# Performance work log

Hardware: AMD Instinct MI355X
Metric: run time of the kernel (lower is better)

## Reference

```python
import jax, jax.numpy as jnp
import numpy as np
from jax import lax

B_SZ, L, D, N, R = 1, 4096, 768, 16, 48  # R = dt_rank = ceil(D/16)


def _soft_clamp(x, lo=1e-4, hi=10.0):
    center = (hi + lo) / 2.0
    half_range = (hi - lo) / 2.0
    return center + half_range * jnp.tanh((x - center) / half_range)


def setup_inputs() -> dict:
    key = jax.random.key(0)
    ks = jax.random.split(key, 6)
    x = jax.random.normal(ks[0], (B_SZ, L, D), jnp.float32)
    # A_log init: log(1..N) broadcast over D (HiPPO-style S4D-real init)
    A_log = jnp.log(jnp.broadcast_to(jnp.arange(1, N + 1, dtype=jnp.float32), (D, N)))
    D_param = jnp.ones((D,), jnp.float32)
    # lecun_normal kernels
    W_bc = jax.random.normal(ks[1], (D, 2 * N), jnp.float32) / np.sqrt(D).astype(np.float32)
    W_dt = jax.random.normal(ks[2], (D, R), jnp.float32) / np.sqrt(D).astype(np.float32)
    W_dtp = jax.random.normal(ks[3], (R, D), jnp.float32) / np.sqrt(R).astype(np.float32)
    # dt bias init: inverse-softplus of uniform(dt_min, dt_max)
    dt = jax.random.uniform(ks[4], (D,), jnp.float32, 0.001, 0.1)
    dt = jnp.clip(dt, 1e-4)
    b_dt = dt + jnp.log(-jnp.expm1(-dt))
    rms_scale = jnp.ones((D,), jnp.float32)  # RMSNorm learnable scale
    return {"x": x, "A_log": A_log, "D_param": D_param, "W_bc": W_bc,
            "W_dt": W_dt, "W_dtp": W_dtp, "b_dt": b_dt, "rms_scale": rms_scale}


def reference(x, A_log, D_param, W_bc, W_dt, W_dtp, b_dt, rms_scale):
    n = A_log.shape[1]
    A = -jnp.exp(A_log)                                   # (D, N)
    bc = x @ W_bc                                         # (B, L, 2N)
    B_sel, C_sel = bc[..., :n], bc[..., n:]               # (B, L, N) each
    # delta = softplus(dt_proj(x_dt)) -> RMSNorm -> soft_clamp  (tustin mode)
    delta = jax.nn.softplus((x @ W_dt) @ W_dtp + b_dt)    # (B, L, D)
    delta = delta * lax.rsqrt(jnp.mean(delta * delta, axis=-1, keepdims=True) + 1e-6) * rms_scale
    delta = _soft_clamp(delta, 1e-4, 10.0)
    # Bilinear (Tustin) discretization, all fp32 already
    dE = delta[..., None]                                 # (B, L, D, 1)
    half = 0.5 * dE * A                                   # (B, L, D, N)
    denom = 1.0 - half
    A_bar = (1.0 + half) / denom                          # (B, L, D, N)
    B_bar = jnp.sqrt(dE) * B_sel[:, :, None, :] / denom   # (B, L, D, N)
    # trapezoidal input averaging
    x_prev = jnp.concatenate([jnp.zeros_like(x[:, :1]), x[:, :-1]], axis=1)
    x_in = 0.5 * (x + x_prev)                             # (B, L, D)
    Bx = B_bar * x_in[..., None]                          # (B, L, D, N)

    def op(left, right):
        a_l, b_l = left
        a_r, b_r = right
        return (a_r * a_l, a_r * b_l + b_r)

    _, all_h = lax.associative_scan(op, (A_bar, Bx), axis=1)
    y = jnp.sum(C_sel[:, :, None, :] * all_h, axis=-1)    # (B, L, D)
    return y + D_param * x
```

## Files before the change

kernel.cpp:

```cpp
#include <hip/hip_runtime.h>
#include <math.h>

#define LSEQ 4096
#define DD 768
#define NST 16
#define RNK 48
#define TCH 64
#define NCH (LSEQ / TCH)
#define KSTEPS 24
#define NTILES 5
#define WFRAG_N (KSTEPS * NTILES * 64 * 8)
#define WDTP_N  (2 * RNK * 64 * 8)

typedef __attribute__((ext_vector_type(8))) short bf16x8;
typedef __attribute__((ext_vector_type(4))) float f32x4;

__device__ __forceinline__ float softplus_f(float z) {
    float e = __expf(-fabsf(z));
    return fmaxf(z, 0.0f) + __logf(1.0f + e);
}

__device__ __forceinline__ float tanh_fast(float w) {
    float t = __expf(2.0f * fabsf(w));
    float r = 1.0f - 2.0f / (t + 1.0f);
    return copysignf(r, w);
}

__device__ __forceinline__ float soft_clamp_f(float v) {
    const float ctr = 5.00005f;
    const float hr  = 4.99995f;
    const float inv_hr = 1.0f / 4.99995f;
    return ctr + hr * tanh_fast((v - ctr) * inv_hr);
}

__device__ __forceinline__ float wave_sum(float v) {
    #pragma unroll
    for (int m = 32; m >= 1; m >>= 1) v += __shfl_xor(v, m, 64);
    return v;
}

__device__ __forceinline__ unsigned short rne_bf16(float v) {
    unsigned u = __float_as_uint(v);
    return (unsigned short)((u + 0x7FFFu + ((u >> 16) & 1u)) >> 16);
}

__global__ __launch_bounds__(256) void k_prep(
    const float* __restrict__ W_dt, const float* __restrict__ W_bc,
    const float* __restrict__ W_dtp,
    unsigned short* __restrict__ wf_hi, unsigned short* __restrict__ wf_lo,
    unsigned short* __restrict__ wp_hi, unsigned short* __restrict__ wp_lo)
{
    int i = blockIdx.x * 256 + threadIdx.x;
    if (i < WFRAG_N) {
        int j  = i & 7;
        int l  = (i >> 3) & 63;
        int nk = i >> 9;
        int n  = nk % NTILES;
        int kk = nk / NTILES;
        int k   = kk * 32 + (l >> 4) * 8 + j;
        int col = n * 16 + (l & 15);
        float v = (col < RNK) ? W_dt[k * RNK + col] : W_bc[k * 32 + (col - RNK)];
        unsigned short h = rne_bf16(v);
        float hf = __uint_as_float((unsigned)h << 16);
        wf_hi[i] = h;
        wf_lo[i] = rne_bf16(v - hf);
    } else if (i < WFRAG_N + WDTP_N) {
        int ii = i - WFRAG_N;
        int j  = ii & 7;
        int l  = (ii >> 3) & 63;
        int nk = ii >> 9;
        int n  = nk % RNK;
        int ks = nk / RNK;
        int k   = ks * 32 + (l >> 4) * 8 + j;
        int col = n * 16 + (l & 15);
        float v = (k < RNK) ? W_dtp[k * DD + col] : 0.f;
        unsigned short h = rne_bf16(v);
        float hf = __uint_as_float((unsigned)h << 16);
        wp_hi[ii] = h;
        wp_lo[ii] = rne_bf16(v - hf);
    }
}

__global__ __launch_bounds__(512) void k_proj_mfma(
    const float* __restrict__ x,
    const unsigned short* __restrict__ wf_hi,
    const unsigned short* __restrict__ wf_lo,
    const unsigned short* __restrict__ wp_hi,
    const unsigned short* __restrict__ wp_lo,
    const float* __restrict__ b_dt, const float* __restrict__ rms_scale,
    float* __restrict__ c0_out, float* __restrict__ c1_out,
    float* __restrict__ bc_out)
{
    __shared__ __align__(16) float smem_x[16 * 772];
    __shared__ __align__(16) float smem_sp[16 * 772];
    __shared__ __align__(16) float t_lds[16][RNK];
    __shared__ float red2[8][16];

    const int tid  = threadIdx.x;
    const int lane = tid & 63;
    const int wq   = tid >> 6;
    const int mt   = blockIdx.x;

    {
        const float4* xg = (const float4*)(x + (size_t)mt * 16 * DD);
        #pragma unroll 2
        for (int idx = tid; idx < 3072; idx += 512) {
            int r = idx / 192, c4 = idx - r * 192;
            *(float4*)&smem_x[r * 772 + c4 * 4] = xg[idx];
        }
    }
    __syncthreads();

    const int rloc = lane & 15;
    const int ko   = (lane >> 4) * 8;

    f32x4 acc[NTILES];
    #pragma unroll
    for (int n = 0; n < NTILES; ++n) acc[n] = (f32x4){0.f, 0.f, 0.f, 0.f};

    #pragma unroll
    for (int k3 = 0; k3 < 3; ++k3) {
        const int kk = wq * 3 + k3;
        const float* xp = &smem_x[rloc * 772 + kk * 32 + ko];
        float4 xa = *(const float4*)xp;
        float4 xb = *(const float4*)(xp + 4);
        float va[8] = {xa.x, xa.y, xa.z, xa.w, xb.x, xb.y, xb.z, xb.w};
        bf16x8 ah, al;
        #pragma unroll
        for (int j = 0; j < 8; ++j) {
            unsigned short h = rne_bf16(va[j]);
            float hf = __uint_as_float((unsigned)h << 16);
            ah[j] = (short)h;
            al[j] = (short)rne_bf16(va[j] - hf);
        }
        const int base = kk * (NTILES * 512) + lane * 8;
        #pragma unroll
        for (int n = 0; n < NTILES; ++n) {
            bf16x8 bh = *(const bf16x8*)(wf_hi + base + n * 512);
            bf16x8 bl = *(const bf16x8*)(wf_lo + base + n * 512);
            acc[n] = __builtin_amdgcn_mfma_f32_16x16x32_bf16(al, bh, acc[n], 0, 0, 0);
            acc[n] = __builtin_amdgcn_mfma_f32_16x16x32_bf16(ah, bl, acc[n], 0, 0, 0);
            acc[n] = __builtin_amdgcn_mfma_f32_16x16x32_bf16(ah, bh, acc[n], 0, 0, 0);
        }
    }
    __syncthreads();

    if (wq > 0) {
        float* red = smem_sp + ((wq - 1) * 64 + lane) * 20;
        #pragma unroll
        for (int n = 0; n < NTILES; ++n)
            #pragma unroll
            for (int r = 0; r < 4; ++r) red[n * 4 + r] = acc[n][r];
    }
    __syncthreads();
    if (wq == 0) {
        #pragma unroll
        for (int w = 0; w < 7; ++w) {
            const float* red = smem_sp + (w * 64 + lane) * 20;
            #pragma unroll
            for (int n = 0; n < NTILES; ++n)
                #pragma unroll
                for (int r = 0; r < 4; ++r) acc[n][r] += red[n * 4 + r];
        }
        const int r0 = (lane >> 4) * 4;
        const int cb = lane & 15;
        #pragma unroll
        for (int n = 0; n < 3; ++n)
            #pragma unroll
            for (int r = 0; r < 4; ++r)
                t_lds[r0 + r][n * 16 + cb] = acc[n][r];
        #pragma unroll
        for (int n = 3; n < 5; ++n)
            #pragma unroll
            for (int r = 0; r < 4; ++r)
                bc_out[(size_t)(mt * 16 + r0 + r) * 32 + (n - 3) * 16 + cb] = acc[n][r];
    }
    __syncthreads();

    bf16x8 tah[2], tal[2];
    #pragma unroll
    for (int ks = 0; ks < 2; ++ks) {
        const int kbase = ks * 32 + ko;
        float tv[8];
        #pragma unroll
        for (int j = 0; j < 8; ++j)
            tv[j] = (kbase + j < RNK) ? t_lds[rloc][kbase + j] : 0.f;
        #pragma unroll
        for (int j = 0; j < 8; ++j) {
            unsigned short h = rne_bf16(tv[j]);
            float hf = __uint_as_float((unsigned)h << 16);
            tah[ks][j] = (short)h;
            tal[ks][j] = (short)rne_bf16(tv[j] - hf);
        }
    }

    const int r0 = (lane >> 4) * 4;
    #pragma unroll
    for (int nn = 0; nn < 6; ++nn) {
        const int n = wq * 6 + nn;
        f32x4 z = (f32x4){0.f, 0.f, 0.f, 0.f};
        {
            const int b0 = n * 512 + lane * 8;
            bf16x8 bh = *(const bf16x8*)(wp_hi + b0);
            bf16x8 bl = *(const bf16x8*)(wp_lo + b0);
            z = __builtin_amdgcn_mfma_f32_16x16x32_bf16(tal[0], bh, z, 0, 0, 0);
            z = __builtin_amdgcn_mfma_f32_16x16x32_bf16(tah[0], bl, z, 0, 0, 0);
            z = __builtin_amdgcn_mfma_f32_16x16x32_bf16(tah[0], bh, z, 0, 0, 0);
        }
        {
            const int b1 = (RNK + n) * 512 + lane * 8;
            bf16x8 bh = *(const bf16x8*)(wp_hi + b1);
            bf16x8 bl = *(const bf16x8*)(wp_lo + b1);
            z = __builtin_amdgcn_mfma_f32_16x16x32_bf16(tal[1], bh, z, 0, 0, 0);
            z = __builtin_amdgcn_mfma_f32_16x16x32_bf16(tah[1], bl, z, 0, 0, 0);
            z = __builtin_amdgcn_mfma_f32_16x16x32_bf16(tah[1], bh, z, 0, 0, 0);
        }
        const int col = n * 16 + (lane & 15);
        const float bb = b_dt[col];
        #pragma unroll
        for (int r = 0; r < 4; ++r)
            smem_sp[(r0 + r) * 772 + col] = softplus_f(z[r] + bb);
    }
    __syncthreads();

    const int d0 = tid;
    const int d1 = tid + 512;
    const bool has2 = (tid < 256);
    {
        float sp0[16], sp1[16];
        #pragma unroll
        for (int li = 0; li < 16; ++li) {
            sp0[li] = smem_sp[li * 772 + d0];
            sp1[li] = has2 ? smem_sp[li * 772 + d1] : 0.f;
        }
        #pragma unroll
        for (int li = 0; li < 16; ++li) {
            float ss = wave_sum(sp0[li] * sp0[li] + sp1[li] * sp1[li]);
            if (lane == 0) red2[wq][li] = ss;
        }
        __syncthreads();
        float rs0 = rms_scale[d0];
        float rs1 = has2 ? rms_scale[d1] : 0.f;
        float xm0 = (mt > 0) ? x[(size_t)(mt * 16 - 1) * DD + d0] : 0.f;
        float xm1 = (has2 && mt > 0) ? x[(size_t)(mt * 16 - 1) * DD + d1] : 0.f;
        #pragma unroll
        for (int li = 0; li < 16; ++li) {
            float tot = 0.f;
            #pragma unroll
            for (int k = 0; k < 8; ++k) tot += red2[k][li];
            float inv = rsqrtf(tot * (1.0f / DD) + 1e-6f);
            size_t rowoff = (size_t)(mt * 16 + li) * DD;

            float dl0 = soft_clamp_f(sp0[li] * inv * rs0);
            float xl0 = smem_x[li * 772 + d0];
            float xp0 = (li == 0) ? xm0 : smem_x[(li - 1) * 772 + d0];
            c0_out[rowoff + d0] = 0.5f * dl0;
            c1_out[rowoff + d0] = sqrtf(dl0) * 0.5f * (xl0 + xp0);

            if (has2) {
                float dl1 = soft_clamp_f(sp1[li] * inv * rs1);
                float xl1 = smem_x[li * 772 + d1];
                float xp1 = (li == 0) ? xm1 : smem_x[(li - 1) * 772 + d1];
                c0_out[rowoff + d1] = 0.5f * dl1;
                c1_out[rowoff + d1] = sqrtf(dl1) * 0.5f * (xl1 + xp1);
            }
        }
    }
}

__global__ __launch_bounds__(256, 4) void k_scan1(
    const float* __restrict__ c0b, const float* __restrict__ c1b,
    const float* __restrict__ bc, const float* __restrict__ A_log,
    float* __restrict__ Pbuf, float* __restrict__ Hbuf)
{
    __shared__ __align__(16) float c0v[TCH * 64];
    __shared__ __align__(16) float c1v[TCH * 64];
    __shared__ __align__(16) float bs[TCH * 16];

    const int tid = threadIdx.x;
    const int db  = blockIdx.x * 64;
    const int c   = blockIdx.y;
    const int l0  = c * TCH;

    for (int i = tid; i < TCH * 16; i += 256) {
        int r = i >> 4, f = i & 15;
        *(float4*)&c0v[r * 64 + f * 4] =
            *(const float4*)&c0b[(size_t)(l0 + r) * DD + db + f * 4];
        *(float4*)&c1v[r * 64 + f * 4] =
            *(const float4*)&c1b[(size_t)(l0 + r) * DD + db + f * 4];
    }
    for (int i = tid; i < TCH * 4; i += 256) {
        int r = i >> 2, f = i & 3;
        *(float4*)&bs[r * 16 + f * 4] =
            *(const float4*)&bc[(size_t)(l0 + r) * 32 + f * 4];
    }

    const int lane = tid & 63;
    const int w    = tid >> 6;
    const int q    = lane >> 4;
    const int dlo  = (lane & 15) + w * 16;
    const int d    = db + dlo;

    float An[4];
    {
        float4 a = *(const float4*)&A_log[d * NST + q * 4];
        An[0] = -__expf(a.x); An[1] = -__expf(a.y);
        An[2] = -__expf(a.z); An[3] = -__expf(a.w);
    }
    __syncthreads();

    float h[4]  = {0.f, 0.f, 0.f, 0.f};
    float Pp[4] = {1.f, 1.f, 1.f, 1.f};

    #pragma unroll 4
    for (int ll = 0; ll < TCH; ++ll) {
        float c0 = c0v[ll * 64 + dlo];
        float c1 = c1v[ll * 64 + dlo];
        float4 Bc = *(const float4*)&bs[ll * 16 + q * 4];

        float dn0 = fmaf(-c0, An[0], 1.0f);
        float dn1 = fmaf(-c0, An[1], 1.0f);
        float dn2 = fmaf(-c0, An[2], 1.0f);
        float dn3 = fmaf(-c0, An[3], 1.0f);
        float m01 = dn0 * dn1, m23 = dn2 * dn3;
        float ip  = __builtin_amdgcn_rcpf(m01 * m23);
        float ip01 = ip * m23, ip23 = ip * m01;
        float iv0 = ip01 * dn1, iv1 = ip01 * dn0;
        float iv2 = ip23 * dn3, iv3 = ip23 * dn2;
        float t10 = 2.0f - dn0, t11 = 2.0f - dn1;
        float t12 = 2.0f - dn2, t13 = 2.0f - dn3;

        Pp[0] *= t10 * iv0;
        Pp[1] *= t11 * iv1;
        Pp[2] *= t12 * iv2;
        Pp[3] *= t13 * iv3;
        h[0] = fmaf(t10, h[0], c1 * Bc.x) * iv0;
        h[1] = fmaf(t11, h[1], c1 * Bc.y) * iv1;
        h[2] = fmaf(t12, h[2], c1 * Bc.z) * iv2;
        h[3] = fmaf(t13, h[3], c1 * Bc.w) * iv3;
    }
    #pragma unroll
    for (int n = 0; n < 4; ++n) {
        int idx = (c * NST + q * 4 + n) * DD + d;
        Pbuf[idx] = Pp[n];
        Hbuf[idx] = h[n];
    }
}

__global__ __launch_bounds__(64) void k_scan2(
    float* __restrict__ Pbuf, const float* __restrict__ Hbuf)
{
    const int s = blockIdx.x * 64 + threadIdx.x;
    const int d = s % DD;
    const int n = s / DD;
    const int stride = NST * DD;

    int idx = n * DD + d;
    int idx_pf = idx;
    float p[8], h[8];
    #pragma unroll
    for (int i = 0; i < 8; ++i) {
        p[i] = Pbuf[idx_pf];
        h[i] = Hbuf[idx_pf];
        idx_pf += stride;
    }

    float carry = 0.f;
    for (int g = 0; g < NCH / 8; ++g) {
        float pn[8], hn[8];
        if (g + 1 < NCH / 8) {
            #pragma unroll
            for (int i = 0; i < 8; ++i) {
                pn[i] = Pbuf[idx_pf];
                hn[i] = Hbuf[idx_pf];
                idx_pf += stride;
            }
        }
        #pragma unroll
        for (int i = 0; i < 8; ++i) {
            Pbuf[idx] = carry;
            carry = fmaf(p[i], carry, h[i]);
            idx += stride;
        }
        #pragma unroll
        for (int i = 0; i < 8; ++i) { p[i] = pn[i]; h[i] = hn[i]; }
    }
}

__global__ __launch_bounds__(256, 4) void k_scan3(
    const float* __restrict__ x, const float* __restrict__ c0b,
    const float* __restrict__ c1b, const float* __restrict__ bc,
    const float* __restrict__ A_log, const float* __restrict__ carryin,
    const float* __restrict__ D_param, float* __restrict__ out)
{
    __shared__ __align__(16) float c0v[TCH * 64];
    __shared__ __align__(16) float c1v[TCH * 64];
    __shared__ __align__(16) float bs[TCH * 32];

    const int tid = threadIdx.x;
    const int db  = blockIdx.x * 64;
    const int c   = blockIdx.y;
    const int l0  = c * TCH;

    for (int i = tid; i < TCH * 16; i += 256) {
        int r = i >> 4, f = i & 15;
        *(float4*)&c0v[r * 64 + f * 4] =
            *(const float4*)&c0b[(size_t)(l0 + r) * DD + db + f * 4];
        *(float4*)&c1v[r * 64 + f * 4] =
            *(const float4*)&c1b[(size_t)(l0 + r) * DD + db + f * 4];
    }
    for (int i = tid; i < TCH * 8; i += 256) {
        int r = i >> 3, f = i & 7;
        *(float4*)&bs[r * 32 + f * 4] =
            *(const float4*)&bc[(size_t)(l0 + r) * 32 + f * 4];
    }

    const int lane = tid & 63;
    const int w    = tid >> 6;
    const int q    = lane >> 4;
    const int dlo  = (lane & 15) + w * 16;
    const int d    = db + dlo;

    float An[4];
    {
        float4 a = *(const float4*)&A_log[d * NST + q * 4];
        An[0] = -__expf(a.x); An[1] = -__expf(a.y);
        An[2] = -__expf(a.z); An[3] = -__expf(a.w);
    }
    float h[4];
    #pragma unroll
    for (int n = 0; n < 4; ++n)
        h[n] = carryin[(c * NST + q * 4 + n) * DD + d];
    const float Dp = D_param[d];

    __syncthreads();

    float xv_n = x[(size_t)l0 * DD + d];
    #pragma unroll 4
    for (int ll = 0; ll < TCH; ++ll) {
        float xv = xv_n;
        const int lnx = (l0 + ll + 1 < LSEQ) ? l0 + ll + 1 : l0 + ll;
        xv_n = x[(size_t)lnx * DD + d];

        float c0 = c0v[ll * 64 + dlo];
        float c1 = c1v[ll * 64 + dlo];
        float4 Bc = *(const float4*)&bs[ll * 32 + q * 4];
        float4 Cc = *(const float4*)&bs[ll * 32 + 16 + q * 4];

        float dn0 = fmaf(-c0, An[0], 1.0f);
        float dn1 = fmaf(-c0, An[1], 1.0f);
        float dn2 = fmaf(-c0, An[2], 1.0f);
        float dn3 = fmaf(-c0, An[3], 1.0f);
        float m01 = dn0 * dn1, m23 = dn2 * dn3;
        float ip  = __builtin_amdgcn_rcpf(m01 * m23);
        float ip01 = ip * m23, ip23 = ip * m01;
        float iv0 = ip01 * dn1, iv1 = ip01 * dn0;
        float iv2 = ip23 * dn3, iv3 = ip23 * dn2;
        float t10 = 2.0f - dn0, t11 = 2.0f - dn1;
        float t12 = 2.0f - dn2, t13 = 2.0f - dn3;

        h[0] = fmaf(t10, h[0], c1 * Bc.x) * iv0;
        h[1] = fmaf(t11, h[1], c1 * Bc.y) * iv1;
        h[2] = fmaf(t12, h[2], c1 * Bc.z) * iv2;
        h[3] = fmaf(t13, h[3], c1 * Bc.w) * iv3;

        float y = h[0] * Cc.x;
        y = fmaf(h[1], Cc.y, y);
        y = fmaf(h[2], Cc.z, y);
        y = fmaf(h[3], Cc.w, y);

        y += __shfl_xor(y, 16, 64);
        y += __shfl_xor(y, 32, 64);
        if (q == 0)
            out[(size_t)(l0 + ll) * DD + d] = fmaf(Dp, xv, y);
    }
}

extern "C" void kernel_launch(void* const* d_in, const int* in_sizes, int n_in,
                              void* d_out, int out_size, void* d_ws, size_t ws_size,
                              hipStream_t stream) {
    const float* x         = (const float*)d_in[0];
    const float* A_log     = (const float*)d_in[1];
    const float* D_param   = (const float*)d_in[2];
    const float* W_bc      = (const float*)d_in[3];
    const float* W_dt      = (const float*)d_in[4];
    const float* W_dtp     = (const float*)d_in[5];
    const float* b_dt      = (const float*)d_in[6];
    const float* rms_scale = (const float*)d_in[7];
    float* out = (float*)d_out;

    float* ws    = (float*)d_ws;
    float* c0buf = ws;
    float* c1buf = c0buf + (size_t)LSEQ * DD;
    float* bcbuf = c1buf + (size_t)LSEQ * DD;
    float* Pbuf  = bcbuf + (size_t)LSEQ * 32;
    float* Hbuf  = Pbuf + (size_t)NCH * NST * DD;
    unsigned short* wf_hi = (unsigned short*)(Hbuf + (size_t)NCH * NST * DD);
    unsigned short* wf_lo = wf_hi + WFRAG_N;
    unsigned short* wp_hi = wf_lo + WFRAG_N;
    unsigned short* wp_lo = wp_hi + WDTP_N;

    k_prep<<<(WFRAG_N + WDTP_N + 255) / 256, 256, 0, stream>>>(
        W_dt, W_bc, W_dtp, wf_hi, wf_lo, wp_hi, wp_lo);
    k_proj_mfma<<<LSEQ / 16, 512, 0, stream>>>(x, wf_hi, wf_lo, wp_hi, wp_lo,
                                               b_dt, rms_scale, c0buf, c1buf,
                                               bcbuf);
    k_scan1<<<dim3(DD / 64, NCH), 256, 0, stream>>>(c0buf, c1buf, bcbuf, A_log,
                                                    Pbuf, Hbuf);
    k_scan2<<<(DD * NST) / 64, 64, 0, stream>>>(Pbuf, Hbuf);
    k_scan3<<<dim3(DD / 64, NCH), 256, 0, stream>>>(x, c0buf, c1buf, bcbuf,
                                                    A_log, Pbuf, D_param, out);
}
```

Measured before the change: 74.62 us.

## Fold chunk-carry scan into final scan kernel, removing separate carry pass

Removes the k_scan2 kernel that sequentially propagated per-chunk carries. Instead, each k_scan3 block recomputes its incoming state by folding all preceding chunk (P, H) summaries from global memory. This saves one kernel launch and the serialized carry pass. In exchange the work becomes quadratic in the chunk count, and late chunks carry a long dependent chain of global loads.

```diff
diff --git a/kernel.cpp b/kernel.cpp
--- a/kernel.cpp
+++ b/kernel.cpp
@@ -347,50 +347,11 @@
     }
 }
 
-__global__ __launch_bounds__(64) void k_scan2(
-    float* __restrict__ Pbuf, const float* __restrict__ Hbuf)
-{
-    const int s = blockIdx.x * 64 + threadIdx.x;
-    const int d = s % DD;
-    const int n = s / DD;
-    const int stride = NST * DD;
-
-    int idx = n * DD + d;
-    int idx_pf = idx;
-    float p[8], h[8];
-    #pragma unroll
-    for (int i = 0; i < 8; ++i) {
-        p[i] = Pbuf[idx_pf];
-        h[i] = Hbuf[idx_pf];
-        idx_pf += stride;
-    }
-
-    float carry = 0.f;
-    for (int g = 0; g < NCH / 8; ++g) {
-        float pn[8], hn[8];
-        if (g + 1 < NCH / 8) {
-            #pragma unroll
-            for (int i = 0; i < 8; ++i) {
-                pn[i] = Pbuf[idx_pf];
-                hn[i] = Hbuf[idx_pf];
-                idx_pf += stride;
-            }
-        }
-        #pragma unroll
-        for (int i = 0; i < 8; ++i) {
-            Pbuf[idx] = carry;
-            carry = fmaf(p[i], carry, h[i]);
-            idx += stride;
-        }
-        #pragma unroll
-        for (int i = 0; i < 8; ++i) { p[i] = pn[i]; h[i] = hn[i]; }
-    }
-}
-
 __global__ __launch_bounds__(256, 4) void k_scan3(
     const float* __restrict__ x, const float* __restrict__ c0b,
     const float* __restrict__ c1b, const float* __restrict__ bc,
-    const float* __restrict__ A_log, const float* __restrict__ carryin,
+    const float* __restrict__ A_log,
+    const float* __restrict__ Pbuf, const float* __restrict__ Hbuf,
     const float* __restrict__ D_param, float* __restrict__ out)
 {
     __shared__ __align__(16) float c0v[TCH * 64];
@@ -427,11 +388,28 @@
         An[0] = -__expf(a.x); An[1] = -__expf(a.y);
         An[2] = -__expf(a.z); An[3] = -__expf(a.w);
     }
-    float h[4];
-    #pragma unroll
-    for (int n = 0; n < 4; ++n)
-        h[n] = carryin[(c * NST + q * 4 + n) * DD + d];
     const float Dp = D_param[d];
+
+    float h[4] = {0.f, 0.f, 0.f, 0.f};
+    {
+        const int stride = NST * DD;
+        int b0 = (q * 4 + 0) * DD + d;
+        int b1 = (q * 4 + 1) * DD + d;
+        int b2 = (q * 4 + 2) * DD + d;
+        int b3 = (q * 4 + 3) * DD + d;
+        int off = 0;
+        for (int cc = 0; cc < c; ++cc) {
+            float p0 = Pbuf[b0 + off], h0 = Hbuf[b0 + off];
+            float p1 = Pbuf[b1 + off], h1 = Hbuf[b1 + off];
+            float p2 = Pbuf[b2 + off], h2 = Hbuf[b2 + off];
+            float p3 = Pbuf[b3 + off], h3 = Hbuf[b3 + off];
+            h[0] = fmaf(p0, h[0], h0);
+            h[1] = fmaf(p1, h[1], h1);
+            h[2] = fmaf(p2, h[2], h2);
+            h[3] = fmaf(p3, h[3], h3);
+            off += stride;
+        }
+    }
 
     __syncthreads();
 
@@ -507,7 +485,7 @@
                                                bcbuf);
     k_scan1<<<dim3(DD / 64, NCH), 256, 0, stream>>>(c0buf, c1buf, bcbuf, A_log,
                                                     Pbuf, Hbuf);
-    k_scan2<<<(DD * NST) / 64, 64, 0, stream>>>(Pbuf, Hbuf);
     k_scan3<<<dim3(DD / 64, NCH), 256, 0, stream>>>(x, c0buf, c1buf, bcbuf,
-                                                    A_log, Pbuf, D_param, out);
-}
+                                                    A_log, Pbuf, Hbuf,
+                                                    D_param, out);
+}
```

Result: slower. 90.34 us (+21.1%).
